# Optimization experiments

Hardware: AMD Instinct MI355X
Metric: run time of the kernel (lower is better)

Reference implementation:

```python
import jax, jax.numpy as jnp
import numpy as np

N_NODES = 50000
N_EDGES = 800000
BN_EPS = 1e-5


def setup_inputs() -> dict:
    key = jax.random.key(0)
    ks = jax.random.split(key, 8)
    feat = jax.random.normal(ks[0], (N_NODES, 512), dtype=jnp.float32)
    src = jax.random.randint(ks[1], (N_EDGES,), 0, N_NODES, dtype=jnp.int32)
    dst = jax.random.randint(ks[2], (N_EDGES,), 0, N_NODES, dtype=jnp.int32)
    W0 = jax.random.normal(ks[3], (512, 128), dtype=jnp.float32) * 0.05
    W1 = jax.random.normal(ks[4], (128, 128), dtype=jnp.float32) * 0.05
    Wp1 = jax.random.normal(ks[5], (128, 256), dtype=jnp.float32) * 0.05
    bp1 = jnp.zeros((256,), dtype=jnp.float32)
    gamma = jnp.ones((256,), dtype=jnp.float32)
    beta = jnp.zeros((256,), dtype=jnp.float32)
    Wp2 = jax.random.normal(ks[6], (256, 128), dtype=jnp.float32) * 0.05
    bp2 = jnp.zeros((128,), dtype=jnp.float32)
    return {"feat": feat, "src": src, "dst": dst, "W0": W0, "W1": W1,
            "Wp1": Wp1, "bp1": bp1, "gamma": gamma, "beta": beta,
            "Wp2": Wp2, "bp2": bp2}


def reference(feat, src, dst, W0, W1, Wp1, bp1, gamma, beta, Wp2, bp2):
    N = feat.shape[0]
    # in-degrees, clamped to >=1, then D^{-1/2}
    deg = jax.ops.segment_sum(jnp.ones_like(dst, dtype=jnp.float32), dst,
                              num_segments=N)
    dinv = jnp.power(jnp.maximum(deg, 1.0), -0.5)[:, None]  # [N,1]

    def low_conv(h):
        # 2h - L_sym h = h + D^{-1/2} A D^{-1/2} h
        scaled = h * dinv
        agg = jax.ops.segment_sum(scaled[src], dst, num_segments=N)
        return h + agg * dinv

    h = low_conv(feat @ W0)      # linear0 (no bias) + conv0
    h = low_conv(h @ W1)         # linear1 (no bias) + conv1

    # MLPHead: Linear -> BatchNorm1d (training stats) -> ReLU -> Linear
    z = h @ Wp1 + bp1
    mu = jnp.mean(z, axis=0)
    var = jnp.mean((z - mu) ** 2, axis=0)  # biased var, torch training mode
    z = (z - mu) * jax.lax.rsqrt(var + BN_EPS) * gamma + beta
    z = jax.nn.relu(z)
    return z @ Wp2 + bp2
```

## Files before the change

### kernel.cpp

```cpp
#include <hip/hip_runtime.h>
#include <math.h>

constexpr int NN  = 50000;
constexpr int NE  = 800000;
constexpr int NNP = 50048;
constexpr int NB  = (NN + 255) / 256;
constexpr int GX  = NNP / 128;
constexpr int FILLB = (NE + 511) / 512;

typedef __bf16 bf16x8 __attribute__((ext_vector_type(8)));
typedef float  f32x4  __attribute__((ext_vector_type(4)));
typedef __attribute__((address_space(1))) unsigned int as1_uint;
typedef __attribute__((address_space(3))) unsigned int as3_uint;

__device__ __forceinline__ unsigned short f2bf(float x) {
    unsigned int u = __float_as_uint(x);
    return (unsigned short)((u + 0x7FFFu + ((u >> 16) & 1u)) >> 16);
}
__device__ __forceinline__ float bf2f(unsigned short h) {
    return __uint_as_float(((unsigned int)h) << 16);
}
__device__ __forceinline__ float rdlanef(float v, int j) {
    return __uint_as_float(__builtin_amdgcn_readlane(__float_as_uint(v), j));
}

__device__ __forceinline__ void gload16(const unsigned short* g, unsigned short* l) {
    __builtin_amdgcn_global_load_lds((const as1_uint*)(unsigned long long)g,
                                     (as3_uint*)(unsigned long long)l, 16, 0, 0);
}

__global__ void k_bsum(const int* __restrict__ cnt, int* __restrict__ bsum) {
    int i = blockIdx.x * 256 + threadIdx.x;
    int v = (i < NN) ? cnt[i] : 0;
#pragma unroll
    for (int off = 32; off; off >>= 1) v += __shfl_down(v, off, 64);
    __shared__ int tmp[4];
    if ((threadIdx.x & 63) == 0) tmp[threadIdx.x >> 6] = v;
    __syncthreads();
    if (threadIdx.x == 0) bsum[blockIdx.x] = tmp[0] + tmp[1] + tmp[2] + tmp[3];
}

__global__ void k_scan_bsum(const int* __restrict__ bsum, int* __restrict__ boff) {
    __shared__ int s[256];
    int t = threadIdx.x;
    int v = (t < NB) ? bsum[t] : 0;
    s[t] = v;
    __syncthreads();
    for (int off = 1; off < 256; off <<= 1) {
        int u = (t >= off) ? s[t - off] : 0;
        __syncthreads();
        s[t] += u;
        __syncthreads();
    }
    if (t < NB) boff[t] = s[t] - v;
}

__global__ void k_scan_block(const int* __restrict__ cnt, const int* __restrict__ boff,
                             int* __restrict__ rowoff, float* __restrict__ dinv) {
    __shared__ int s[256];
    int t = threadIdx.x;
    int i = blockIdx.x * 256 + t;
    int v = (i < NN) ? cnt[i] : 0;
    s[t] = v;
    __syncthreads();
    for (int off = 1; off < 256; off <<= 1) {
        int u = (t >= off) ? s[t - off] : 0;
        __syncthreads();
        s[t] += u;
        __syncthreads();
    }
    if (i < NN) {
        rowoff[i] = boff[blockIdx.x] + s[t] - v;
        dinv[i] = rsqrtf(fmaxf((float)v, 1.0f));
    }
}

__global__ __launch_bounds__(256) void k_gather_shfl(
    const unsigned short* __restrict__ HH, const float* __restrict__ dinv,
    const int* __restrict__ rowoff, const int* __restrict__ cnt,
    const int* __restrict__ eidx, unsigned short* __restrict__ OH)
{
    int node = blockIdx.x * 4 + (threadIdx.x >> 6);
    int lane = threadIdx.x & 63;
    if (node >= NNP) return;
    size_t rb = (size_t)node * 128 + lane * 2;
    if (node >= NN) {
        *reinterpret_cast<ushort2*>(&OH[rb]) = make_ushort2(0, 0);
        return;
    }
    int beg = rowoff[node], n = cnt[node];
    int c2 = lane * 2;
    float ax = 0.f, ay = 0.f;
    for (int jj = 0; jj < n; jj += 64) {
        int m = min(n - jj, 64);
        int el = (lane < m) ? eidx[beg + jj + lane] : 0;
        float dl = dinv[el];
        int mp = (m + 7) & ~7;
        for (int j = 0; j < mp; j += 8) {
            int ss[8]; float dd[8]; ushort2 vv[8];
#pragma unroll
            for (int q = 0; q < 8; ++q) {
                int jq = (j + q) & 63;
                ss[q] = __builtin_amdgcn_readlane(el, jq);
                dd[q] = (j + q < m) ? rdlanef(dl, jq) : 0.f;
            }
#pragma unroll
            for (int q = 0; q < 8; ++q)
                vv[q] = *reinterpret_cast<const ushort2*>(&HH[(size_t)ss[q] * 128 + c2]);
#pragma unroll
            for (int q = 0; q < 8; ++q) {
                ax = fmaf(bf2f(vv[q].x), dd[q], ax);
                ay = fmaf(bf2f(vv[q].y), dd[q], ay);
            }
        }
    }
    float d = dinv[node];
    ushort2 sh = *reinterpret_cast<const ushort2*>(&HH[rb]);
    float hx = fmaf(ax, d, bf2f(sh.x));
    float hy = fmaf(ay, d, bf2f(sh.y));
    *reinterpret_cast<ushort2*>(&OH[rb]) = make_ushort2(f2bf(hx), f2bf(hy));
}

__global__ void k_wprep_count(const float* __restrict__ W0, const float* __restrict__ W1,
                              const float* __restrict__ Wp1, const float* __restrict__ Wp2,
                              unsigned short* __restrict__ W0t, unsigned short* __restrict__ W1pt,
                              unsigned short* __restrict__ Wp2t, float* __restrict__ stats,
                              const int* __restrict__ dst, int* __restrict__ cnt,
                              int* __restrict__ pos) {
    int b = blockIdx.x, t = threadIdx.x;
    if (b >= 512) {
        int i = (b - 512) * 256 + t;
        if (i < NE) pos[i] = atomicAdd(&cnt[dst[i]], 1);
        return;
    }
    if (b < 128) {
        if (b < 2) stats[b * 256 + t] = 0.f;
        float s = 0.f;
        for (int k = 0; k < 128; ++k) s = fmaf(W1[b * 128 + k], Wp1[k * 256 + t], s);
        W1pt[t * 128 + b] = f2bf(s);
    } else if (b < 384) {
        int idx = (b - 128) * 256 + t;
        int k = idx >> 7, n = idx & 127;
        W0t[n * 512 + k] = f2bf(W0[idx]);
    } else {
        int idx = (b - 384) * 256 + t;
        int k = idx >> 7, n = idx & 127;
        Wp2t[n * 256 + k] = f2bf(Wp2[idx]);
    }
}

__global__ __launch_bounds__(512) void k_gemm1_fill(
    const float* __restrict__ Af, const unsigned short* __restrict__ BH,
    unsigned short* __restrict__ OHs,
    const int* __restrict__ src, const int* __restrict__ dst,
    const int* __restrict__ rowoff, const int* __restrict__ pos,
    int* __restrict__ eidx)
{
    if (blockIdx.x >= GX) {
        int e = (blockIdx.x - GX) * 512 + threadIdx.x;
        if (e < NE) {
            int d = dst[e];
            eidx[rowoff[d] + pos[e]] = src[e];
        }
        return;
    }
    constexpr int K = 512, NCOLS = 128;
    __shared__ __align__(16) unsigned short lds[2 * 4096];
    unsigned short* ldsA = lds;
    unsigned short* ldsB = lds + 4096;

    const int tid  = threadIdx.x;
    const int lane = tid & 63;
    const int wid  = tid >> 6;
    const int wm   = wid >> 1;
    const int wn   = wid & 1;
    const int row0 = blockIdx.x * 128;

    const int srow  = tid >> 2;
    const int skg   = tid & 3;
    const int skswz = skg ^ ((srow >> 1) & 3);
    const size_t aSrc = (size_t)(row0 + srow) * K + skswz * 8;
    const size_t bSrc = (size_t)srow * K + skswz * 8;

    const int frow = lane & 15;
    const int fkg  = lane >> 4;

    f32x4 acc[2][4] = {};

    for (int k0 = 0; k0 < K; k0 += 32) {
        float4 f0, f1;
        if (row0 + srow < NN) {
            const float* ap = Af + aSrc + k0;
            f0 = *reinterpret_cast<const float4*>(ap);
            f1 = *reinterpret_cast<const float4*>(ap + 4);
        } else {
            f0 = make_float4(0.f, 0.f, 0.f, 0.f);
            f1 = f0;
        }
        uint4 w;
        w.x = (unsigned)f2bf(f0.x) | ((unsigned)f2bf(f0.y) << 16);
        w.y = (unsigned)f2bf(f0.z) | ((unsigned)f2bf(f0.w) << 16);
        w.z = (unsigned)f2bf(f1.x) | ((unsigned)f2bf(f1.y) << 16);
        w.w = (unsigned)f2bf(f1.z) | ((unsigned)f2bf(f1.w) << 16);
        *reinterpret_cast<uint4*>(&ldsA[tid * 8]) = w;
        gload16(BH + bSrc + k0, ldsB + tid * 8);
        __syncthreads();

        bf16x8 a_h[2], b_h[4];
#pragma unroll
        for (int mi = 0; mi < 2; ++mi) {
            int ar  = wm * 32 + mi * 16 + frow;
            int idx = ar * 32 + ((fkg ^ ((ar >> 1) & 3)) * 8);
            a_h[mi] = *reinterpret_cast<const bf16x8*>(&ldsA[idx]);
        }
#pragma unroll
        for (int ni = 0; ni < 4; ++ni) {
            int bc  = wn * 64 + ni * 16 + frow;
            int idx = bc * 32 + ((fkg ^ ((bc >> 1) & 3)) * 8);
            b_h[ni] = *reinterpret_cast<const bf16x8*>(&ldsB[idx]);
        }
#pragma unroll
        for (int mi = 0; mi < 2; ++mi)
#pragma unroll
            for (int ni = 0; ni < 4; ++ni)
                acc[mi][ni] = __builtin_amdgcn_mfma_f32_16x16x32_bf16(a_h[mi], b_h[ni], acc[mi][ni], 0, 0, 0);
        __syncthreads();
    }

#pragma unroll
    for (int mi = 0; mi < 2; ++mi) {
        int rbase = row0 + wm * 32 + mi * 16 + (lane >> 4) * 4;
#pragma unroll
        for (int ni = 0; ni < 4; ++ni) {
            int col = wn * 64 + ni * 16 + (lane & 15);
#pragma unroll
            for (int r = 0; r < 4; ++r)
                OHs[(size_t)(rbase + r) * NCOLS + col] = f2bf(acc[mi][ni][r]);
        }
    }
}

template <int K, int NCOLS, bool BIAS, int AMODE, int OMODE, bool STATS>
__global__ __launch_bounds__(512) void k_mfma(
    const unsigned short* __restrict__ AH, const unsigned short* __restrict__ BH,
    const float* __restrict__ bias,
    const float* __restrict__ stats, const float* __restrict__ gamma,
    const float* __restrict__ beta,
    float* __restrict__ C, unsigned short* __restrict__ OHs,
    float* __restrict__ statsOut)
{
    __shared__ __align__(16) unsigned short lds[2 * 4096];
    unsigned short* ldsA = lds;
    unsigned short* ldsB = lds + 4096;

    const int tid  = threadIdx.x;
    const int lane = tid & 63;
    const int wid  = tid >> 6;
    const int wm   = wid >> 1;
    const int wn   = wid & 1;
    const int row0 = blockIdx.x * 128;
    const int col0 = blockIdx.y * 128;

    const int srow  = tid >> 2;
    const int skg   = tid & 3;
    const int skswz = skg ^ ((srow >> 1) & 3);
    const size_t aSrc = (size_t)(row0 + srow) * K + skswz * 8;
    const size_t bSrc = (size_t)(col0 + srow) * K + skswz * 8;

    const int frow = lane & 15;
    const int fkg  = lane >> 4;

    __shared__ float s_scl[256], s_shf[256];
    if constexpr (AMODE == 2) {
        if (tid < K) {
            float mu  = stats[tid] * (1.0f / NN);
            float var = stats[256 + tid] * (1.0f / NN) - mu * mu;
            float s = gamma[tid] * rsqrtf(var + 1e-5f);
            s_scl[tid] = s;
            s_shf[tid] = beta[tid] - mu * s;
        }
        __syncthreads();
    }

    f32x4 acc[2][4] = {};

    for (int k0 = 0; k0 < K; k0 += 32) {
        if constexpr (AMODE == 2) {
            uint4 raw = *reinterpret_cast<const uint4*>(&AH[aSrc + k0]);
            unsigned rw[4] = {raw.x, raw.y, raw.z, raw.w};
            int kc = k0 + skswz * 8;
            float vv[8];
#pragma unroll
            for (int q = 0; q < 8; ++q) {
                float z = bf2f((unsigned short)((q & 1) ? (rw[q >> 1] >> 16)
                                                        : (rw[q >> 1] & 0xFFFF)));
                vv[q] = fmaxf(fmaf(z, s_scl[kc + q], s_shf[kc + q]), 0.f);
            }
            uint4 w;
            w.x = (unsigned)f2bf(vv[0]) | ((unsigned)f2bf(vv[1]) << 16);
            w.y = (unsigned)f2bf(vv[2]) | ((unsigned)f2bf(vv[3]) << 16);
            w.z = (unsigned)f2bf(vv[4]) | ((unsigned)f2bf(vv[5]) << 16);
            w.w = (unsigned)f2bf(vv[6]) | ((unsigned)f2bf(vv[7]) << 16);
            *reinterpret_cast<uint4*>(&ldsA[tid * 8]) = w;
        } else {
            gload16(AH + aSrc + k0, ldsA + tid * 8);
        }
        gload16(BH + bSrc + k0, ldsB + tid * 8);
        __syncthreads();

        bf16x8 a_h[2], b_h[4];
#pragma unroll
        for (int mi = 0; mi < 2; ++mi) {
            int ar  = wm * 32 + mi * 16 + frow;
            int idx = ar * 32 + ((fkg ^ ((ar >> 1) & 3)) * 8);
            a_h[mi] = *reinterpret_cast<const bf16x8*>(&ldsA[idx]);
        }
#pragma unroll
        for (int ni = 0; ni < 4; ++ni) {
            int bc  = wn * 64 + ni * 16 + frow;
            int idx = bc * 32 + ((fkg ^ ((bc >> 1) & 3)) * 8);
            b_h[ni] = *reinterpret_cast<const bf16x8*>(&ldsB[idx]);
        }
#pragma unroll
        for (int mi = 0; mi < 2; ++mi)
#pragma unroll
            for (int ni = 0; ni < 4; ++ni)
                acc[mi][ni] = __builtin_amdgcn_mfma_f32_16x16x32_bf16(a_h[mi], b_h[ni], acc[mi][ni], 0, 0, 0);
        __syncthreads();
    }

    float psum[4] = {0.f, 0.f, 0.f, 0.f}, psq[4] = {0.f, 0.f, 0.f, 0.f};
#pragma unroll
    for (int mi = 0; mi < 2; ++mi) {
        int rbase = row0 + wm * 32 + mi * 16 + (lane >> 4) * 4;
#pragma unroll
        for (int ni = 0; ni < 4; ++ni) {
            int col = col0 + wn * 64 + ni * 16 + (lane & 15);
            float b = BIAS ? bias[col] : 0.f;
#pragma unroll
            for (int r = 0; r < 4; ++r) {
                int row = rbase + r;
                float v = acc[mi][ni][r] + b;
                if constexpr (STATS) {
                    if (row < NN) { psum[ni] += v; psq[ni] = fmaf(v, v, psq[ni]); }
                }
                if constexpr (OMODE == 1) {
                    OHs[(size_t)row * NCOLS + col] = f2bf(v);
                } else {
                    if (row < NN) C[(size_t)row * NCOLS + col] = v;
                }
            }
        }
    }

    if constexpr (STATS) {
        __shared__ float s_sum[128], s_sq[128];
        if (tid < 128) { s_sum[tid] = 0.f; s_sq[tid] = 0.f; }
        __syncthreads();
#pragma unroll
        for (int ni = 0; ni < 4; ++ni) {
            float a = psum[ni], q = psq[ni];
            a += __shfl_xor(a, 16); a += __shfl_xor(a, 32);
            q += __shfl_xor(q, 16); q += __shfl_xor(q, 32);
            if ((lane >> 4) == 0) {
                int cl = wn * 64 + ni * 16 + lane;
                atomicAdd(&s_sum[cl], a);
                atomicAdd(&s_sq[cl], q);
            }
        }
        __syncthreads();
        if (tid < 128) {
            atomicAdd(&statsOut[col0 + tid], s_sum[tid]);
            atomicAdd(&statsOut[256 + col0 + tid], s_sq[tid]);
        }
    }
}

extern "C" void kernel_launch(void* const* d_in, const int* in_sizes, int n_in,
                              void* d_out, int out_size, void* d_ws, size_t ws_size,
                              hipStream_t stream) {
    const float* feat  = (const float*)d_in[0];
    const int*   src   = (const int*)d_in[1];
    const int*   dst   = (const int*)d_in[2];
    const float* W0    = (const float*)d_in[3];
    const float* W1    = (const float*)d_in[4];
    const float* Wp1   = (const float*)d_in[5];
    const float* bp1   = (const float*)d_in[6];
    const float* gamma = (const float*)d_in[7];
    const float* beta  = (const float*)d_in[8];
    const float* Wp2   = (const float*)d_in[9];
    const float* bp2   = (const float*)d_in[10];
    float* out = (float*)d_out;

    char* wsb = (char*)d_ws;
    float* dinv   = (float*)(wsb + 4ull * 0);
    int*   cnt    = (int*)  (wsb + 4ull * 50048);
    int*   rowoff = (int*)  (wsb + 4ull * 100096);
    int*   bsum   = (int*)  (wsb + 4ull * 150144);
    int*   boff   = (int*)  (wsb + 4ull * 150400);
    int*   pos    = (int*)  (wsb + 4ull * 150656);
    int*   eidx   = (int*)  (wsb + 4ull * 950656);
    float* stats  = (float*)(wsb + 4ull * 1750656);
    unsigned short* W0t  = (unsigned short*)(wsb + 4ull * 1751168);
    unsigned short* W1pt = W0t + 65536;
    unsigned short* Wp2t = W1pt + 32768;
    unsigned short* H0 = (unsigned short*)(wsb + 4ull * 1816704);
    unsigned short* h1 = (unsigned short*)(wsb + 4ull * 5019776);
    unsigned short* h2 = H0;
    unsigned short* ZH = (unsigned short*)(wsb + 4ull * 8222848);

    hipMemsetAsync(cnt, 0, 50048 * sizeof(int), stream);
    k_wprep_count<<<512 + (NE + 255) / 256, 256, 0, stream>>>(
        W0, W1, Wp1, Wp2, W0t, W1pt, Wp2t, stats, dst, cnt, pos);
    k_bsum<<<NB, 256, 0, stream>>>(cnt, bsum);
    k_scan_bsum<<<1, 256, 0, stream>>>(bsum, boff);
    k_scan_block<<<NB, 256, 0, stream>>>(cnt, boff, rowoff, dinv);

    k_gemm1_fill<<<GX + FILLB, 512, 0, stream>>>(
        feat, W0t, H0, src, dst, rowoff, pos, eidx);

    k_gather_shfl<<<NNP / 4, 256, 0, stream>>>(H0, dinv, rowoff, cnt, eidx, h1);
    k_gather_shfl<<<NNP / 4, 256, 0, stream>>>(h1, dinv, rowoff, cnt, eidx, h2);

    k_mfma<128, 256, true, 0, 1, true><<<dim3(GX, 2), 512, 0, stream>>>(
        h2, W1pt, bp1, nullptr, nullptr, nullptr, nullptr, ZH, stats);

    k_mfma<256, 128, true, 2, 0, false><<<dim3(GX, 1), 512, 0, stream>>>(
        ZH, Wp2t, bp2, stats, gamma, beta, out, nullptr, nullptr);
}
```

Measured before the change: 197.1 us.

## Replace random CSR scatter with two-pass bucketed fill via staging buffer

The edge-index fill, which used to scatter each src directly into eidx at random positions, now runs in two passes. First, each chunk of 4096 edges is locally bucketed by destination node range (256-node buckets) into a staging buffer, with per-chunk bucket offsets. A new kernel then walks each bucket's segments across all chunks and writes into eidx, so the writes land in a localized region. This aims to improve write locality of the scatter, at the cost of an extra kernel launch, extra staging traffic (8 bytes per edge written and read) and LDS atomics.

```diff
diff --git a/kernel.cpp b/kernel.cpp
--- a/kernel.cpp
+++ b/kernel.cpp
@@ -6,7 +6,9 @@
 constexpr int NNP = 50048;
 constexpr int NB  = (NN + 255) / 256;
 constexpr int GX  = NNP / 128;
-constexpr int FILLB = (NE + 511) / 512;
+constexpr int CHUNK = 4096;
+constexpr int NCH   = (NE + CHUNK - 1) / CHUNK;
+constexpr int NBK2  = 196;
 
 typedef __bf16 bf16x8 __attribute__((ext_vector_type(8)));
 typedef float  f32x4  __attribute__((ext_vector_type(4)));
@@ -154,13 +156,48 @@
     unsigned short* __restrict__ OHs,
     const int* __restrict__ src, const int* __restrict__ dst,
     const int* __restrict__ rowoff, const int* __restrict__ pos,
-    int* __restrict__ eidx)
+    int2* __restrict__ staging, int* __restrict__ starts)
 {
+    const int tid = threadIdx.x;
     if (blockIdx.x >= GX) {
-        int e = (blockIdx.x - GX) * 512 + threadIdx.x;
-        if (e < NE) {
-            int d = dst[e];
-            eidx[rowoff[d] + pos[e]] = src[e];
+        __shared__ int cntb[256], scanb[256], cnt2b[256];
+        int c = blockIdx.x - GX;
+        int base = c * CHUNK;
+        if (tid < 256) { cntb[tid] = 0; cnt2b[tid] = 0; }
+        __syncthreads();
+        int bloc[8], floc[8], sloc[8];
+#pragma unroll
+        for (int q = 0; q < 8; ++q) {
+            int e = base + q * 512 + tid;
+            if (e < NE) {
+                int d = dst[e];
+                bloc[q] = d >> 8;
+                floc[q] = rowoff[d] + pos[e];
+                sloc[q] = src[e];
+                atomicAdd(&cntb[bloc[q]], 1);
+            } else bloc[q] = -1;
+        }
+        __syncthreads();
+        if (tid < 256) scanb[tid] = cntb[tid];
+        __syncthreads();
+        for (int off = 1; off < 256; off <<= 1) {
+            int u = 0;
+            if (tid < 256 && tid >= off) u = scanb[tid - off];
+            __syncthreads();
+            if (tid < 256) scanb[tid] += u;
+            __syncthreads();
+        }
+        if (tid < 197) {
+            int ex = (tid < 196) ? (scanb[tid] - cntb[tid]) : scanb[195];
+            starts[c * 197 + tid] = ex;
+        }
+        __syncthreads();
+#pragma unroll
+        for (int q = 0; q < 8; ++q) {
+            if (bloc[q] >= 0) {
+                int slot = (scanb[bloc[q]] - cntb[bloc[q]]) + atomicAdd(&cnt2b[bloc[q]], 1);
+                staging[(size_t)base + slot] = make_int2(floc[q], sloc[q]);
+            }
         }
         return;
     }
@@ -169,7 +206,6 @@
     unsigned short* ldsA = lds;
     unsigned short* ldsB = lds + 4096;
 
-    const int tid  = threadIdx.x;
     const int lane = tid & 63;
     const int wid  = tid >> 6;
     const int wm   = wid >> 1;
@@ -236,6 +272,29 @@
 #pragma unroll
             for (int r = 0; r < 4; ++r)
                 OHs[(size_t)(rbase + r) * NCOLS + col] = f2bf(acc[mi][ni][r]);
+        }
+    }
+}
+
+__global__ __launch_bounds__(256) void k_fill2(
+    const int2* __restrict__ staging, const int* __restrict__ starts,
+    int* __restrict__ eidx)
+{
+    int b    = blockIdx.x >> 1;
+    int half = blockIdx.x & 1;
+    int tid  = threadIdx.x;
+    int wv   = tid >> 6, lane = tid & 63;
+    __shared__ int sS[NCH], sE[NCH];
+    for (int c = tid; c < NCH; c += 256) {
+        sS[c] = starts[c * 197 + b];
+        sE[c] = starts[c * 197 + b + 1];
+    }
+    __syncthreads();
+    for (int c = half * 4 + wv; c < NCH; c += 8) {
+        int s = sS[c], e = sE[c];
+        for (int i = s + lane; i < e; i += 64) {
+            int2 r = staging[(size_t)c * CHUNK + i];
+            eidx[r.x] = r.y;
         }
     }
 }
@@ -401,13 +460,15 @@
     int*   pos    = (int*)  (wsb + 4ull * 150656);
     int*   eidx   = (int*)  (wsb + 4ull * 950656);
     float* stats  = (float*)(wsb + 4ull * 1750656);
-    unsigned short* W0t  = (unsigned short*)(wsb + 4ull * 1751168);
+    int*   starts = (int*)  (wsb + 4ull * 1751168);
+    unsigned short* W0t  = (unsigned short*)(wsb + 4ull * 1789824);
     unsigned short* W1pt = W0t + 65536;
     unsigned short* Wp2t = W1pt + 32768;
-    unsigned short* H0 = (unsigned short*)(wsb + 4ull * 1816704);
-    unsigned short* h1 = (unsigned short*)(wsb + 4ull * 5019776);
+    int2*  staging = (int2*)(wsb + 4ull * 1855360);
+    unsigned short* H0 = (unsigned short*)(wsb + 4ull * 3460992);
+    unsigned short* h1 = (unsigned short*)(wsb + 4ull * 6664064);
     unsigned short* h2 = H0;
-    unsigned short* ZH = (unsigned short*)(wsb + 4ull * 8222848);
+    unsigned short* ZH = (unsigned short*)(wsb + 4ull * 9867136);
 
     hipMemsetAsync(cnt, 0, 50048 * sizeof(int), stream);
     k_wprep_count<<<512 + (NE + 255) / 256, 256, 0, stream>>>(
@@ -416,8 +477,10 @@
     k_scan_bsum<<<1, 256, 0, stream>>>(bsum, boff);
     k_scan_block<<<NB, 256, 0, stream>>>(cnt, boff, rowoff, dinv);
 
-    k_gemm1_fill<<<GX + FILLB, 512, 0, stream>>>(
-        feat, W0t, H0, src, dst, rowoff, pos, eidx);
+    k_gemm1_fill<<<GX + NCH, 512, 0, stream>>>(
+        feat, W0t, H0, src, dst, rowoff, pos, staging, starts);
+
+    k_fill2<<<2 * NBK2, 256, 0, stream>>>(staging, starts, eidx);
 
     k_gather_shfl<<<NNP / 4, 256, 0, stream>>>(H0, dinv, rowoff, cnt, eidx, h1);
     k_gather_shfl<<<NNP / 4, 256, 0, stream>>>(h1, dinv, rowoff, cnt, eidx, h2);
```

After: 204.8 us. +3.9%, slower.
